# Kernel tuning notes

Hardware: AMD Instinct MI355X
Metric: run time of the kernel (lower is better)

Reference implementation:

```python
import jax, jax.numpy as jnp
import numpy as np

GROUPS = 32
EPS = 1e-5

def group_norm(x, w, b):
    # x: [B, C, T]
    B, C, T = x.shape
    g = x.reshape(B, GROUPS, C // GROUPS, T)
    mu = g.mean(axis=(2, 3), keepdims=True)
    var = g.var(axis=(2, 3), keepdims=True)
    g = (g - mu) * jax.lax.rsqrt(var + EPS)
    return g.reshape(B, C, T) * w[None, :, None] + b[None, :, None]

def conv1x1(x, w, b):
    # x: [B, C, T], w: [O, C], b: [O]
    return jnp.einsum('oc,bct->bot', w, x) + b[None, :, None]

def setup_inputs() -> dict:
    key = jax.random.key(0)
    ks = jax.random.split(key, 10)
    B, C, H, W = 128, 512, 16, 16
    d = {}
    d['criminal_cond'] = jax.random.normal(ks[0], (B, C, H, W), jnp.float32)
    d['morph_cond'] = jax.random.normal(ks[1], (B, C, H, W), jnp.float32)
    d['norm_w'] = jax.random.uniform(ks[2], (C,), jnp.float32, 0.5, 1.5)
    d['norm_b'] = 0.02 * jax.random.normal(ks[3], (C,), jnp.float32)
    d['qkv_w'] = jax.random.normal(ks[4], (3 * C, C), jnp.float32) / np.sqrt(C)
    d['qkv_b'] = 0.02 * jax.random.normal(ks[5], (3 * C,), jnp.float32)
    d['ekv_w'] = jax.random.normal(ks[6], (2 * C, C), jnp.float32) / np.sqrt(C)
    d['ekv_b'] = 0.02 * jax.random.normal(ks[7], (2 * C,), jnp.float32)
    d['proj_w'] = jax.random.normal(ks[8], (C, C), jnp.float32) / np.sqrt(C)
    d['proj_b'] = 0.02 * jax.random.normal(ks[9], (C,), jnp.float32)
    return d

def reference(criminal_cond, morph_cond, norm_w, norm_b, qkv_w, qkv_b, ekv_w, ekv_b, proj_w, proj_b):
    B, C, H, W = criminal_cond.shape
    x = criminal_cond.reshape(B, C, H * W)          # [B, C, T]
    cond = morph_cond.reshape(B, C, H * W)          # [B, C, S], S == T here
    h = group_norm(x, norm_w, norm_b)
    qkv = conv1x1(h, qkv_w, qkv_b)                  # [B, 3C, T]
    q, k, v = jnp.split(qkv, 3, axis=1)
    ekv = conv1x1(cond, ekv_w, ekv_b)               # [B, 2C, S]
    ek, ev = jnp.split(ekv, 2, axis=1)
    k = jnp.concatenate([ek, k], axis=-1)           # [B, C, S+T]
    v = jnp.concatenate([ev, v], axis=-1)
    scale = 1.0 / np.sqrt(np.sqrt(C))               # single head, head_dim = C
    logits = jnp.einsum('bct,bcs->bts', q * scale, k * scale)
    w = jax.nn.softmax(logits, axis=-1)             # [B, T, S+T]
    a = jnp.einsum('bts,bcs->bct', w, v)            # [B, C, T]
    hout = conv1x1(a, proj_w, proj_b)
    attn_out = (x + hout).reshape(B, C, H, W)
    return 2.0 * morph_cond - attn_out
```

## Files before the change

kernel.cpp:

```cpp
#include <hip/hip_runtime.h>
#include <hip/hip_bf16.h>
#include <math.h>

#define NB 128
#define NC 512
#define NT 256
#define NL 512
#define NG 32
#define SCALE2 0.04419417382415922f

typedef __attribute__((ext_vector_type(8))) short bf16x8;
typedef __attribute__((ext_vector_type(4))) float f32x4;
typedef __attribute__((ext_vector_type(4))) unsigned short u16x4;
typedef __attribute__((ext_vector_type(8))) unsigned short u16x8;
typedef __hip_bfloat16 bf16;

struct Params {
  const float *x, *morph, *qkvb, *ekvb, *projb;
  const bf16 *wq, *we, *wp;
  bf16 *hT, *mT, *qT, *kfT, *vf;
  float *out;
  int b0;
};

enum { M_QKV = 0, M_EKV = 1 };

__device__ inline unsigned short f2bf_bits(float f) {
  bf16 h = __float2bfloat16(f);
  return *reinterpret_cast<unsigned short*>(&h);
}

__device__ inline void gld16(const void* g, void* lds) {
  __builtin_amdgcn_global_load_lds(
      (const __attribute__((address_space(1))) unsigned int*)g,
      (__attribute__((address_space(3))) unsigned int*)lds, 16, 0, 0);
}

__global__ __launch_bounds__(256) void gn_stats_k(const float* __restrict__ x,
                                                  float* __restrict__ stats) {
  const int bg = blockIdx.x;
  const float4* p4 = (const float4*)(x + (size_t)bg * 4096);
  float s = 0.f, s2 = 0.f;
  #pragma unroll
  for (int i = 0; i < 4; ++i) {
    float4 v = p4[threadIdx.x + i * 256];
    s  += v.x + v.y + v.z + v.w;
    s2 += v.x * v.x + v.y * v.y + v.z * v.z + v.w * v.w;
  }
  #pragma unroll
  for (int off = 32; off; off >>= 1) {
    s  += __shfl_down(s, off);
    s2 += __shfl_down(s2, off);
  }
  __shared__ float red[8];
  const int wave = threadIdx.x >> 6, lane = threadIdx.x & 63;
  if (lane == 0) { red[wave * 2] = s; red[wave * 2 + 1] = s2; }
  __syncthreads();
  if (threadIdx.x == 0) {
    float S = 0.f, S2 = 0.f;
    for (int w = 0; w < 4; ++w) { S += red[w * 2]; S2 += red[w * 2 + 1]; }
    float mu = S * (1.0f / 4096.0f);
    float var = S2 * (1.0f / 4096.0f) - mu * mu;
    stats[bg * 2]     = mu;
    stats[bg * 2 + 1] = rsqrtf(var + 1e-5f);
  }
}

__global__ __launch_bounds__(256) void cvt_k(const float* __restrict__ s,
                                             bf16* __restrict__ d, int n) {
  int i = blockIdx.x * 256 + threadIdx.x;
  if (i < n) d[i] = __float2bfloat16(s[i]);
}

__global__ __launch_bounds__(256) void transpose2_k(const float* __restrict__ x,
                                                    const float* __restrict__ morph,
                                                    bf16* __restrict__ hT,
                                                    bf16* __restrict__ mT,
                                                    const float* __restrict__ stats,
                                                    const float* __restrict__ gnw,
                                                    const float* __restrict__ gnb,
                                                    int b0, int nbc) {
  __shared__ float sm[64][65];
  const int z = blockIdx.z;
  const int norm = (z < nbc) ? 1 : 0;
  const int lb = norm ? z : z - nbc;
  const int gb = b0 + lb;
  const float* src = norm ? x : morph;
  bf16* dst = norm ? hT : mT;
  const int t0 = blockIdx.x * 64, c0 = blockIdx.y * 64;
  const int tx = threadIdx.x & 15, ty = threadIdx.x >> 4;
  #pragma unroll
  for (int ci = 0; ci < 4; ++ci) {
    const int c = ty + ci * 16;
    const int cg = c0 + c;
    float4 v = *(const float4*)&src[((size_t)gb * NC + cg) * NT + t0 + tx * 4];
    if (norm) {
      float mu = stats[(gb * NG + (cg >> 4)) * 2];
      float rs = stats[(gb * NG + (cg >> 4)) * 2 + 1];
      float wv = gnw[cg], bv = gnb[cg];
      v.x = (v.x - mu) * rs * wv + bv;
      v.y = (v.y - mu) * rs * wv + bv;
      v.z = (v.z - mu) * rs * wv + bv;
      v.w = (v.w - mu) * rs * wv + bv;
    }
    sm[c][tx * 4 + 0] = v.x; sm[c][tx * 4 + 1] = v.y;
    sm[c][tx * 4 + 2] = v.z; sm[c][tx * 4 + 3] = v.w;
  }
  __syncthreads();
  const int t = threadIdx.x >> 2, cq = threadIdx.x & 3;
  u16x8 pk0, pk1;
  #pragma unroll
  for (int k = 0; k < 8; ++k) pk0[k] = f2bf_bits(sm[cq * 16 + k][t]);
  #pragma unroll
  for (int k = 0; k < 8; ++k) pk1[k] = f2bf_bits(sm[cq * 16 + 8 + k][t]);
  bf16* d = dst + ((size_t)lb * NT + t0 + t) * NC + c0 + cq * 16;
  *(u16x8*)d = pk0;
  *(u16x8*)(d + 8) = pk1;
}

template <int MODE>
__global__ __launch_bounds__(256) void gemm_k(Params P) {
  __shared__ unsigned short As[128][32];
  __shared__ unsigned short Bs[128][32];
  const int lb = blockIdx.x;
  const int m0 = blockIdx.y * 128;
  const int n0 = blockIdx.z * 128;
  const int tid = threadIdx.x;
  const int lane = tid & 63, w = tid >> 6;
  const int wr = w >> 1, wc = w & 1;
  const int ln = lane & 15, kq = lane >> 4;

  const bf16 *Ab, *Bb;
  if (MODE == M_QKV) { Ab = P.hT + (size_t)lb * NT * NC; Bb = P.wq; }
  else               { Ab = P.mT + (size_t)lb * NT * NC; Bb = P.we; }

  const char* Abase = (const char*)(Ab + (size_t)m0 * 512);
  const char* Bbase = (const char*)(Bb + (size_t)n0 * 512);

  const int r_lo = w * 32 + (lane >> 2);
  const int cid16 = (lane & 3) * 16;

  f32x4 acc[4][4] = {};

  for (int k0 = 0; k0 < 512; k0 += 32) {
    const size_t kb = (size_t)k0 * 2 + cid16;
    #pragma unroll
    for (int h = 0; h < 2; ++h) {
      const int rw = r_lo + h * 16;
      gld16(Abase + (size_t)rw * 1024 + kb, (char*)As + w * 2048 + h * 1024);
      gld16(Bbase + (size_t)rw * 1024 + kb, (char*)Bs + w * 2048 + h * 1024);
    }
    __syncthreads();
    bf16x8 af[4], bfr[4];
    #pragma unroll
    for (int i = 0; i < 4; ++i)
      af[i] = *(const bf16x8*)&As[wr * 64 + i * 16 + ln][kq * 8];
    #pragma unroll
    for (int j = 0; j < 4; ++j)
      bfr[j] = *(const bf16x8*)&Bs[wc * 64 + j * 16 + ln][kq * 8];
    #pragma unroll
    for (int i = 0; i < 4; ++i)
      #pragma unroll
      for (int j = 0; j < 4; ++j)
        acc[i][j] = __builtin_amdgcn_mfma_f32_16x16x32_bf16(af[i], bfr[j], acc[i][j], 0, 0, 0);
    __syncthreads();
  }

  #pragma unroll
  for (int i = 0; i < 4; ++i) {
    const int ig = m0 + wr * 64 + i * 16 + kq * 4;
    #pragma unroll
    for (int j = 0; j < 4; ++j) {
      const int jg = n0 + wc * 64 + j * 16 + ln;
      f32x4 a = acc[i][j];
      if (MODE == M_QKV) {
        float bias = P.qkvb[jg];
        if (jg < 512) {
          bf16* d = P.qT + ((size_t)lb * NT + ig) * NC + jg;
          #pragma unroll
          for (int r = 0; r < 4; ++r) d[(size_t)r * NC] = __float2bfloat16(a[r] + bias);
        } else if (jg < 1024) {
          bf16* d = P.kfT + ((size_t)lb * NL + 256 + ig) * NC + (jg - 512);
          #pragma unroll
          for (int r = 0; r < 4; ++r) d[(size_t)r * NC] = __float2bfloat16(a[r] + bias);
        } else {
          u16x4 pk;
          #pragma unroll
          for (int r = 0; r < 4; ++r) pk[r] = f2bf_bits(a[r] + bias);
          *(u16x4*)(P.vf + ((size_t)lb * NC + (jg - 1024)) * NL + 256 + ig) = pk;
        }
      } else {
        float bias = P.ekvb[jg];
        if (jg < 512) {
          bf16* d = P.kfT + ((size_t)lb * NL + ig) * NC + jg;
          #pragma unroll
          for (int r = 0; r < 4; ++r) d[(size_t)r * NC] = __float2bfloat16(a[r] + bias);
        } else {
          u16x4 pk;
          #pragma unroll
          for (int r = 0; r < 4; ++r) pk[r] = f2bf_bits(a[r] + bias);
          *(u16x4*)(P.vf + ((size_t)lb * NC + (jg - 512)) * NL + ig) = pk;
        }
      }
    }
  }
}

__global__ __launch_bounds__(256) void attn_k(Params P) {
  __shared__ unsigned short Pbuf[32][520];
  __shared__ float redm[4][32];
  __shared__ float reds[4][32];

  const int lb = blockIdx.x, gb = P.b0 + lb;
  const int t0 = blockIdx.y * 32;
  const int tid = threadIdx.x;
  const int lane = tid & 63, w = tid >> 6;
  const int ln = lane & 15, kq = lane >> 4;

  const bf16* qg  = P.qT  + ((size_t)lb * NT + t0) * NC;
  const bf16* kg  = P.kfT + (size_t)lb * NL * NC;
  const bf16* vg  = P.vf  + (size_t)lb * NC * NL;
  const bf16* wpg = P.wp;

  f32x4 sa[2][8] = {};
  bf16x8 af[2], bfr[8];

  {
    const bf16* qa0 = qg + (size_t)ln * NC + kq * 8;
    const bf16* kb0 = kg + (size_t)(w * 128 + ln) * NC + kq * 8;
    for (int k0 = 0; k0 < 512; k0 += 32) {
      af[0] = *(const bf16x8*)(qa0 + k0);
      af[1] = *(const bf16x8*)(qa0 + (size_t)16 * NC + k0);
      #pragma unroll
      for (int j = 0; j < 8; ++j)
        bfr[j] = *(const bf16x8*)(kb0 + (size_t)j * 16 * NC + k0);
      #pragma unroll
      for (int i = 0; i < 2; ++i)
        #pragma unroll
        for (int j = 0; j < 8; ++j)
          sa[i][j] = __builtin_amdgcn_mfma_f32_16x16x32_bf16(af[i], bfr[j], sa[i][j], 0, 0, 0);
    }
  }

  float mx[2][4], sum[2][4], inv[2][4];
  #pragma unroll
  for (int i = 0; i < 2; ++i)
    #pragma unroll
    for (int r = 0; r < 4; ++r) {
      float m = -1e30f;
      #pragma unroll
      for (int j = 0; j < 8; ++j) m = fmaxf(m, sa[i][j][r]);
      mx[i][r] = m;
    }
  #pragma unroll
  for (int off = 1; off < 16; off <<= 1)
    #pragma unroll
    for (int i = 0; i < 2; ++i)
      #pragma unroll
      for (int r = 0; r < 4; ++r) mx[i][r] = fmaxf(mx[i][r], __shfl_xor(mx[i][r], off));
  if (ln == 0)
    #pragma unroll
    for (int i = 0; i < 2; ++i)
      #pragma unroll
      for (int r = 0; r < 4; ++r) redm[w][i * 16 + kq * 4 + r] = mx[i][r];
  __syncthreads();
  #pragma unroll
  for (int i = 0; i < 2; ++i)
    #pragma unroll
    for (int r = 0; r < 4; ++r) {
      const int row = i * 16 + kq * 4 + r;
      mx[i][r] = fmaxf(fmaxf(redm[0][row], redm[1][row]),
                       fmaxf(redm[2][row], redm[3][row]));
      sum[i][r] = 0.f;
    }
  #pragma unroll
  for (int i = 0; i < 2; ++i)
    #pragma unroll
    for (int j = 0; j < 8; ++j)
      #pragma unroll
      for (int r = 0; r < 4; ++r) {
        float e = __expf(SCALE2 * (sa[i][j][r] - mx[i][r]));
        sa[i][j][r] = e;
        sum[i][r] += e;
      }
  #pragma unroll
  for (int off = 1; off < 16; off <<= 1)
    #pragma unroll
    for (int i = 0; i < 2; ++i)
      #pragma unroll
      for (int r = 0; r < 4; ++r) sum[i][r] += __shfl_xor(sum[i][r], off);
  if (ln == 0)
    #pragma unroll
    for (int i = 0; i < 2; ++i)
      #pragma unroll
      for (int r = 0; r < 4; ++r) reds[w][i * 16 + kq * 4 + r] = sum[i][r];
  __syncthreads();
  #pragma unroll
  for (int i = 0; i < 2; ++i)
    #pragma unroll
    for (int r = 0; r < 4; ++r) {
      const int row = i * 16 + kq * 4 + r;
      inv[i][r] = 1.0f / (reds[0][row] + reds[1][row] + reds[2][row] + reds[3][row]);
    }
  #pragma unroll
  for (int i = 0; i < 2; ++i)
    #pragma unroll
    for (int j = 0; j < 8; ++j)
      #pragma unroll
      for (int r = 0; r < 4; ++r)
        Pbuf[i * 16 + kq * 4 + r][w * 128 + j * 16 + ln] = f2bf_bits(sa[i][j][r] * inv[i][r]);
  __syncthreads();

  f32x4 oa[2][8] = {};
  {
    const bf16* vb0 = vg + (size_t)(w * 128 + ln) * NL + kq * 8;
    for (int k0 = 0; k0 < 512; k0 += 32) {
      af[0] = *(const bf16x8*)&Pbuf[ln][k0 + kq * 8];
      af[1] = *(const bf16x8*)&Pbuf[16 + ln][k0 + kq * 8];
      #pragma unroll
      for (int j = 0; j < 8; ++j)
        bfr[j] = *(const bf16x8*)(vb0 + (size_t)j * 16 * NL + k0);
      #pragma unroll
      for (int i = 0; i < 2; ++i)
        #pragma unroll
        for (int j = 0; j < 8; ++j)
          oa[i][j] = __builtin_amdgcn_mfma_f32_16x16x32_bf16(af[i], bfr[j], oa[i][j], 0, 0, 0);
    }
  }
  __syncthreads();

  #pragma unroll
  for (int i = 0; i < 2; ++i)
    #pragma unroll
    for (int j = 0; j < 8; ++j)
      #pragma unroll
      for (int r = 0; r < 4; ++r)
        Pbuf[i * 16 + kq * 4 + r][w * 128 + j * 16 + ln] = f2bf_bits(oa[i][j][r]);
  __syncthreads();

  f32x4 za[2][8] = {};
  {
    const bf16* wb0 = wpg + (size_t)(w * 128 + ln) * NC + kq * 8;
    for (int k0 = 0; k0 < 512; k0 += 32) {
      af[0] = *(const bf16x8*)&Pbuf[ln][k0 + kq * 8];
      af[1] = *(const bf16x8*)&Pbuf[16 + ln][k0 + kq * 8];
      #pragma unroll
      for (int j = 0; j < 8; ++j)
        bfr[j] = *(const bf16x8*)(wb0 + (size_t)j * 16 * NC + k0);
      #pragma unroll
      for (int i = 0; i < 2; ++i)
        #pragma unroll
        for (int j = 0; j < 8; ++j)
          za[i][j] = __builtin_amdgcn_mfma_f32_16x16x32_bf16(af[i], bfr[j], za[i][j], 0, 0, 0);
    }
  }

  #pragma unroll
  for (int i = 0; i < 2; ++i) {
    const int trow = t0 + i * 16 + kq * 4;
    #pragma unroll
    for (int j = 0; j < 8; ++j) {
      const int c = w * 128 + j * 16 + ln;
      const float bias = P.projb[c];
      const size_t idx = ((size_t)gb * NC + c) * NT + trow;
      float4 mo = *(const float4*)&P.morph[idx];
      float4 xx = *(const float4*)&P.x[idx];
      f32x4 o;
      o[0] = 2.0f * mo.x - xx.x - (za[i][j][0] + bias);
      o[1] = 2.0f * mo.y - xx.y - (za[i][j][1] + bias);
      o[2] = 2.0f * mo.z - xx.z - (za[i][j][2] + bias);
      o[3] = 2.0f * mo.w - xx.w - (za[i][j][3] + bias);
      *(f32x4*)&P.out[idx] = o;
    }
  }
}

extern "C" void kernel_launch(void* const* d_in, const int* in_sizes, int n_in,
                              void* d_out, int out_size, void* d_ws, size_t ws_size,
                              hipStream_t stream) {
  const float* x     = (const float*)d_in[0];
  const float* morph = (const float*)d_in[1];
  const float* gnw   = (const float*)d_in[2];
  const float* gnb   = (const float*)d_in[3];
  const float* qkvw  = (const float*)d_in[4];
  const float* qkvb  = (const float*)d_in[5];
  const float* ekvw  = (const float*)d_in[6];
  const float* ekvb  = (const float*)d_in[7];
  const float* projw = (const float*)d_in[8];
  const float* projb = (const float*)d_in[9];

  bf16* wq = (bf16*)d_ws;
  bf16* we = wq + 786432;
  bf16* wp = we + 524288;
  float* stats = (float*)(wp + 262144);
  bf16* pb = (bf16*)(stats + 8192);

  const size_t per_b = 917504;
  const size_t fixed = (size_t)(786432 + 524288 + 262144) * 2 + 8192 * 4;
  int nbc = NB;
  while (nbc > 1 && fixed + (size_t)nbc * per_b * 2 > ws_size) nbc >>= 1;

  Params P;
  P.x = x; P.morph = morph; P.qkvb = qkvb; P.ekvb = ekvb; P.projb = projb;
  P.wq = wq; P.we = we; P.wp = wp;
  P.hT  = pb;  pb += (size_t)nbc * 131072;
  P.mT  = pb;  pb += (size_t)nbc * 131072;
  P.qT  = pb;  pb += (size_t)nbc * 131072;
  P.kfT = pb;  pb += (size_t)nbc * 262144;
  P.vf  = pb;
  P.out = (float*)d_out;

  gn_stats_k<<<dim3(NB * NG), dim3(256), 0, stream>>>(x, stats);
  cvt_k<<<dim3(3072), dim3(256), 0, stream>>>(qkvw, wq, 786432);
  cvt_k<<<dim3(2048), dim3(256), 0, stream>>>(ekvw, we, 524288);
  cvt_k<<<dim3(1024), dim3(256), 0, stream>>>(projw, wp, 262144);

  for (int b0 = 0; b0 < NB; b0 += nbc) {
    P.b0 = b0;
    transpose2_k<<<dim3(4, 8, 2 * nbc), dim3(256), 0, stream>>>(
        x, morph, P.hT, P.mT, stats, gnw, gnb, b0, nbc);
    gemm_k<M_QKV><<<dim3(nbc, 2, 12), dim3(256), 0, stream>>>(P);
    gemm_k<M_EKV><<<dim3(nbc, 2, 8),  dim3(256), 0, stream>>>(P);
    attn_k       <<<dim3(nbc, 8),     dim3(256), 0, stream>>>(P);
  }
}
```

Before: 602.2 us.

## Split fused attention into LDS-tiled GEMM kernels plus separate softmax

Replaces the single fused attention kernel with three launches of a templated 128x128 LDS-tiled MFMA GEMM: QK^T, P·V, and the output projection. A standalone row-wise softmax kernel sits between the first two GEMMs. The fused kernel streamed K, V and Wp from global memory per wave without LDS staging; the tiled GEMMs share operands across waves and give larger, more regular tiles. In exchange, the fp32 logits and the intermediate P and O make a round trip through global memory, reusing the scratch buffers, and the change adds extra launches and synchronisation points.

```diff
diff --git a/kernel.cpp b/kernel.cpp
--- a/kernel.cpp
+++ b/kernel.cpp
@@ -206,173 +206,113 @@
   }
 }
 
-__global__ __launch_bounds__(256) void attn_k(Params P) {
-  __shared__ unsigned short Pbuf[32][520];
-  __shared__ float redm[4][32];
-  __shared__ float reds[4][32];
-
-  const int lb = blockIdx.x, gb = P.b0 + lb;
-  const int t0 = blockIdx.y * 32;
+template <int MODE>
+__global__ __launch_bounds__(256) void gemm_att(Params P) {
+  __shared__ unsigned short As[128][32];
+  __shared__ unsigned short Bs[128][32];
+  const int lb = blockIdx.x;
+  const int m0 = blockIdx.y * 128;
+  const int n0 = blockIdx.z * 128;
   const int tid = threadIdx.x;
   const int lane = tid & 63, w = tid >> 6;
+  const int wr = w >> 1, wc = w & 1;
   const int ln = lane & 15, kq = lane >> 4;
 
-  const bf16* qg  = P.qT  + ((size_t)lb * NT + t0) * NC;
-  const bf16* kg  = P.kfT + (size_t)lb * NL * NC;
-  const bf16* vg  = P.vf  + (size_t)lb * NC * NL;
-  const bf16* wpg = P.wp;
-
-  f32x4 sa[2][8] = {};
-  bf16x8 af[2], bfr[8];
-
-  {
-    const bf16* qa0 = qg + (size_t)ln * NC + kq * 8;
-    const bf16* kb0 = kg + (size_t)(w * 128 + ln) * NC + kq * 8;
-    for (int k0 = 0; k0 < 512; k0 += 32) {
-      af[0] = *(const bf16x8*)(qa0 + k0);
-      af[1] = *(const bf16x8*)(qa0 + (size_t)16 * NC + k0);
+  const bf16 *Ab, *Bb;
+  if (MODE == 0)      { Ab = P.qT  + (size_t)lb * 131072; Bb = P.kfT + (size_t)lb * NL * NC; }
+  else if (MODE == 1) { Ab = P.qT  + (size_t)lb * 131072; Bb = P.vf  + (size_t)lb * NC * NL; }
+  else                { Ab = P.kfT + (size_t)lb * 262144; Bb = P.wp; }
+
+  const char* Abase = (const char*)(Ab + (size_t)m0 * 512);
+  const char* Bbase = (const char*)(Bb + (size_t)n0 * 512);
+
+  const int r_lo = w * 32 + (lane >> 2);
+  const int cid16 = (lane & 3) * 16;
+
+  f32x4 acc[4][4] = {};
+
+  for (int k0 = 0; k0 < 512; k0 += 32) {
+    const size_t kb = (size_t)k0 * 2 + cid16;
+    #pragma unroll
+    for (int h = 0; h < 2; ++h) {
+      const int rw = r_lo + h * 16;
+      gld16(Abase + (size_t)rw * 1024 + kb, (char*)As + w * 2048 + h * 1024);
+      gld16(Bbase + (size_t)rw * 1024 + kb, (char*)Bs + w * 2048 + h * 1024);
+    }
+    __syncthreads();
+    bf16x8 af[4], bfr[4];
+    #pragma unroll
+    for (int i = 0; i < 4; ++i)
+      af[i] = *(const bf16x8*)&As[wr * 64 + i * 16 + ln][kq * 8];
+    #pragma unroll
+    for (int j = 0; j < 4; ++j)
+      bfr[j] = *(const bf16x8*)&Bs[wc * 64 + j * 16 + ln][kq * 8];
+    #pragma unroll
+    for (int i = 0; i < 4; ++i)
       #pragma unroll
-      for (int j = 0; j < 8; ++j)
-        bfr[j] = *(const bf16x8*)(kb0 + (size_t)j * 16 * NC + k0);
-      #pragma unroll
-      for (int i = 0; i < 2; ++i)
+      for (int j = 0; j < 4; ++j)
+        acc[i][j] = __builtin_amdgcn_mfma_f32_16x16x32_bf16(af[i], bfr[j], acc[i][j], 0, 0, 0);
+    __syncthreads();
+  }
+
+  float* Sg = (float*)P.hT + (size_t)lb * 131072;
+  bf16*  Og = P.kfT + (size_t)lb * 262144;
+  const int gb = P.b0 + lb;
+
+  #pragma unroll
+  for (int i = 0; i < 4; ++i) {
+    const int ig = m0 + wr * 64 + i * 16 + kq * 4;
+    #pragma unroll
+    for (int j = 0; j < 4; ++j) {
+      const int jg = n0 + wc * 64 + j * 16 + ln;
+      f32x4 a = acc[i][j];
+      if (MODE == 0) {
         #pragma unroll
-        for (int j = 0; j < 8; ++j)
-          sa[i][j] = __builtin_amdgcn_mfma_f32_16x16x32_bf16(af[i], bfr[j], sa[i][j], 0, 0, 0);
-    }
-  }
-
-  float mx[2][4], sum[2][4], inv[2][4];
-  #pragma unroll
-  for (int i = 0; i < 2; ++i)
-    #pragma unroll
-    for (int r = 0; r < 4; ++r) {
-      float m = -1e30f;
-      #pragma unroll
-      for (int j = 0; j < 8; ++j) m = fmaxf(m, sa[i][j][r]);
-      mx[i][r] = m;
-    }
-  #pragma unroll
-  for (int off = 1; off < 16; off <<= 1)
-    #pragma unroll
-    for (int i = 0; i < 2; ++i)
-      #pragma unroll
-      for (int r = 0; r < 4; ++r) mx[i][r] = fmaxf(mx[i][r], __shfl_xor(mx[i][r], off));
-  if (ln == 0)
-    #pragma unroll
-    for (int i = 0; i < 2; ++i)
-      #pragma unroll
-      for (int r = 0; r < 4; ++r) redm[w][i * 16 + kq * 4 + r] = mx[i][r];
-  __syncthreads();
-  #pragma unroll
-  for (int i = 0; i < 2; ++i)
-    #pragma unroll
-    for (int r = 0; r < 4; ++r) {
-      const int row = i * 16 + kq * 4 + r;
-      mx[i][r] = fmaxf(fmaxf(redm[0][row], redm[1][row]),
-                       fmaxf(redm[2][row], redm[3][row]));
-      sum[i][r] = 0.f;
-    }
-  #pragma unroll
-  for (int i = 0; i < 2; ++i)
-    #pragma unroll
-    for (int j = 0; j < 8; ++j)
-      #pragma unroll
-      for (int r = 0; r < 4; ++r) {
-        float e = __expf(SCALE2 * (sa[i][j][r] - mx[i][r]));
-        sa[i][j][r] = e;
-        sum[i][r] += e;
+        for (int r = 0; r < 4; ++r) Sg[(size_t)(ig + r) * NL + jg] = a[r];
+      } else if (MODE == 1) {
+        bf16* d = Og + (size_t)ig * NC + jg;
+        #pragma unroll
+        for (int r = 0; r < 4; ++r) d[(size_t)r * NC] = __float2bfloat16(a[r]);
+      } else {
+        const float bias = P.projb[jg];
+        const size_t idx = ((size_t)gb * NC + jg) * NT + ig;
+        float4 mo = *(const float4*)&P.morph[idx];
+        float4 xx = *(const float4*)&P.x[idx];
+        f32x4 o;
+        o[0] = 2.0f * mo.x - xx.x - (a[0] + bias);
+        o[1] = 2.0f * mo.y - xx.y - (a[1] + bias);
+        o[2] = 2.0f * mo.z - xx.z - (a[2] + bias);
+        o[3] = 2.0f * mo.w - xx.w - (a[3] + bias);
+        *(f32x4*)&P.out[idx] = o;
       }
-  #pragma unroll
-  for (int off = 1; off < 16; off <<= 1)
-    #pragma unroll
-    for (int i = 0; i < 2; ++i)
-      #pragma unroll
-      for (int r = 0; r < 4; ++r) sum[i][r] += __shfl_xor(sum[i][r], off);
-  if (ln == 0)
-    #pragma unroll
-    for (int i = 0; i < 2; ++i)
-      #pragma unroll
-      for (int r = 0; r < 4; ++r) reds[w][i * 16 + kq * 4 + r] = sum[i][r];
-  __syncthreads();
-  #pragma unroll
-  for (int i = 0; i < 2; ++i)
-    #pragma unroll
-    for (int r = 0; r < 4; ++r) {
-      const int row = i * 16 + kq * 4 + r;
-      inv[i][r] = 1.0f / (reds[0][row] + reds[1][row] + reds[2][row] + reds[3][row]);
-    }
-  #pragma unroll
-  for (int i = 0; i < 2; ++i)
-    #pragma unroll
-    for (int j = 0; j < 8; ++j)
-      #pragma unroll
-      for (int r = 0; r < 4; ++r)
-        Pbuf[i * 16 + kq * 4 + r][w * 128 + j * 16 + ln] = f2bf_bits(sa[i][j][r] * inv[i][r]);
-  __syncthreads();
-
-  f32x4 oa[2][8] = {};
-  {
-    const bf16* vb0 = vg + (size_t)(w * 128 + ln) * NL + kq * 8;
-    for (int k0 = 0; k0 < 512; k0 += 32) {
-      af[0] = *(const bf16x8*)&Pbuf[ln][k0 + kq * 8];
-      af[1] = *(const bf16x8*)&Pbuf[16 + ln][k0 + kq * 8];
-      #pragma unroll
-      for (int j = 0; j < 8; ++j)
-        bfr[j] = *(const bf16x8*)(vb0 + (size_t)j * 16 * NL + k0);
-      #pragma unroll
-      for (int i = 0; i < 2; ++i)
-        #pragma unroll
-        for (int j = 0; j < 8; ++j)
-          oa[i][j] = __builtin_amdgcn_mfma_f32_16x16x32_bf16(af[i], bfr[j], oa[i][j], 0, 0, 0);
-    }
-  }
-  __syncthreads();
-
-  #pragma unroll
-  for (int i = 0; i < 2; ++i)
-    #pragma unroll
-    for (int j = 0; j < 8; ++j)
-      #pragma unroll
-      for (int r = 0; r < 4; ++r)
-        Pbuf[i * 16 + kq * 4 + r][w * 128 + j * 16 + ln] = f2bf_bits(oa[i][j][r]);
-  __syncthreads();
-
-  f32x4 za[2][8] = {};
-  {
-    const bf16* wb0 = wpg + (size_t)(w * 128 + ln) * NC + kq * 8;
-    for (int k0 = 0; k0 < 512; k0 += 32) {
-      af[0] = *(const bf16x8*)&Pbuf[ln][k0 + kq * 8];
-      af[1] = *(const bf16x8*)&Pbuf[16 + ln][k0 + kq * 8];
-      #pragma unroll
-      for (int j = 0; j < 8; ++j)
-        bfr[j] = *(const bf16x8*)(wb0 + (size_t)j * 16 * NC + k0);
-      #pragma unroll
-      for (int i = 0; i < 2; ++i)
-        #pragma unroll
-        for (int j = 0; j < 8; ++j)
-          za[i][j] = __builtin_amdgcn_mfma_f32_16x16x32_bf16(af[i], bfr[j], za[i][j], 0, 0, 0);
-    }
-  }
-
-  #pragma unroll
-  for (int i = 0; i < 2; ++i) {
-    const int trow = t0 + i * 16 + kq * 4;
-    #pragma unroll
-    for (int j = 0; j < 8; ++j) {
-      const int c = w * 128 + j * 16 + ln;
-      const float bias = P.projb[c];
-      const size_t idx = ((size_t)gb * NC + c) * NT + trow;
-      float4 mo = *(const float4*)&P.morph[idx];
-      float4 xx = *(const float4*)&P.x[idx];
-      f32x4 o;
-      o[0] = 2.0f * mo.x - xx.x - (za[i][j][0] + bias);
-      o[1] = 2.0f * mo.y - xx.y - (za[i][j][1] + bias);
-      o[2] = 2.0f * mo.z - xx.z - (za[i][j][2] + bias);
-      o[3] = 2.0f * mo.w - xx.w - (za[i][j][3] + bias);
-      *(f32x4*)&P.out[idx] = o;
-    }
-  }
+    }
+  }
+}
+
+__global__ __launch_bounds__(256) void softmax_k(Params P) {
+  const int row = blockIdx.x * 4 + (threadIdx.x >> 6);
+  const int lane = threadIdx.x & 63;
+  const int lb = row >> 8, t = row & 255;
+  const float* src = (const float*)P.hT + (size_t)lb * 131072 + (size_t)t * NL + lane * 8;
+  f32x4 a0 = ((const f32x4*)src)[0];
+  f32x4 a1 = ((const f32x4*)src)[1];
+  float v[8] = {a0[0], a0[1], a0[2], a0[3], a1[0], a1[1], a1[2], a1[3]};
+  float m = v[0];
+  #pragma unroll
+  for (int k = 1; k < 8; ++k) m = fmaxf(m, v[k]);
+  #pragma unroll
+  for (int off = 1; off < 64; off <<= 1) m = fmaxf(m, __shfl_xor(m, off));
+  float e[8], s = 0.f;
+  #pragma unroll
+  for (int k = 0; k < 8; ++k) { e[k] = __expf(SCALE2 * (v[k] - m)); s += e[k]; }
+  #pragma unroll
+  for (int off = 1; off < 64; off <<= 1) s += __shfl_xor(s, off);
+  const float inv = 1.0f / s;
+  u16x8 pk;
+  #pragma unroll
+  for (int k = 0; k < 8; ++k) pk[k] = f2bf_bits(e[k] * inv);
+  bf16* dst = P.qT + (size_t)lb * 131072 + (size_t)t * NL + lane * 8;
+  *(u16x8*)dst = pk;
 }
 
 extern "C" void kernel_launch(void* const* d_in, const int* in_sizes, int n_in,
@@ -421,6 +361,9 @@
         x, morph, P.hT, P.mT, stats, gnw, gnb, b0, nbc);
     gemm_k<M_QKV><<<dim3(nbc, 2, 12), dim3(256), 0, stream>>>(P);
     gemm_k<M_EKV><<<dim3(nbc, 2, 8),  dim3(256), 0, stream>>>(P);
-    attn_k       <<<dim3(nbc, 8),     dim3(256), 0, stream>>>(P);
-  }
-}
+    gemm_att<0>  <<<dim3(nbc, 2, 4),  dim3(256), 0, stream>>>(P);
+    softmax_k    <<<dim3(nbc * 64),   dim3(256), 0, stream>>>(P);
+    gemm_att<1>  <<<dim3(nbc, 2, 4),  dim3(256), 0, stream>>>(P);
+    gemm_att<2>  <<<dim3(nbc, 2, 4),  dim3(256), 0, stream>>>(P);
+  }
+}
```

Measured after the change: 542.1 us. 1.11x faster.
